# Performance work log

Measured on AMD Instinct MI355X. Metric: run time of the kernel, lower is better.

## Reference

```python
import jax, jax.numpy as jnp
import numpy as np

B, F, O = 4096, 16384, 256
MANTISSA_BITS = 23  # flip only mantissa bits to keep values finite


def setup_inputs() -> dict:
    key = jax.random.key(0)
    k1, k2, k3, k4 = jax.random.split(key, 4)
    x = jax.random.normal(k1, (B, F), dtype=jnp.float32)
    W = jax.random.normal(k2, (F, O), dtype=jnp.float32) * 0.02
    b = jnp.zeros((O,), dtype=jnp.float32)
    bitswap_coeff = jnp.ones((), dtype=jnp.float32)  # scalar 'bitswap_coeff' weight
    # uniform categorical over flattened features == uniform randint
    idx = jax.random.randint(k3, (B,), 0, F, dtype=jnp.int32)
    bit_positions = jax.random.randint(k4, (B,), 0, MANTISSA_BITS, dtype=jnp.int32)
    return {"x": x, "W": W, "b": b, "bitswap_coeff": bitswap_coeff,
            "idx": idx, "bit_positions": bit_positions}


def _bit_flip(g, bit_positions):
    # SimulateSwap: flip one mantissa bit of the float32 representation
    gi = jax.lax.bitcast_convert_type(g, jnp.int32)
    gi = gi ^ (jnp.int32(1) << bit_positions)
    return jax.lax.bitcast_convert_type(gi, jnp.float32)


def reference(x, W, b, bitswap_coeff, idx, bit_positions):
    rows = jnp.arange(x.shape[0])
    # gather_nd(batch_dims=1): one element per batch row
    g = x[rows, idx]                              # [B]
    updates = _bit_flip(g, bit_positions) - g     # swap_sim(x) - x
    # tensor_scatter_nd_update onto zeros, scaled by bitswap coefficient
    pert = jnp.zeros_like(x).at[rows, idx].set(updates) * bitswap_coeff
    # wrapped layer: Dense
    return (x + pert) @ W + b
```

## Files before the change

### kernel.cpp

```cpp
#include <hip/hip_runtime.h>

#define M_DIM 4096
#define K_DIM 16384
#define N_DIM 256

typedef __bf16 bf16x8 __attribute__((ext_vector_type(8)));
typedef float f32x4 __attribute__((ext_vector_type(4)));
typedef unsigned short us4 __attribute__((ext_vector_type(4)));
typedef unsigned short us8 __attribute__((ext_vector_type(8)));

__device__ __forceinline__ unsigned short f2bf(float f) {
  unsigned int u = __float_as_uint(f);
  u += 0x7fffu + ((u >> 16) & 1u);
  return (unsigned short)(u >> 16);
}

__global__ __launch_bounds__(256) void wt_kernel(const float* __restrict__ W,
                                                 unsigned short* __restrict__ Wt) {
  __shared__ float tile[64][65];
  const int k0 = blockIdx.x * 64, n0 = blockIdx.y * 64;
  const int t = threadIdx.x;
#pragma unroll
  for (int r = 0; r < 4; ++r) {
    int idx4 = r * 256 + t;
    int kr = idx4 >> 4, c4 = idx4 & 15;
    f32x4 v = *(const f32x4*)(W + (size_t)(k0 + kr) * N_DIM + n0 + c4 * 4);
#pragma unroll
    for (int j = 0; j < 4; ++j) tile[kr][c4 * 4 + j] = v[j];
  }
  __syncthreads();
#pragma unroll
  for (int r = 0; r < 4; ++r) {
    int nr = (t >> 4) + r * 16, k4 = t & 15;
    us4 o;
#pragma unroll
    for (int j = 0; j < 4; ++j) o[j] = f2bf(tile[k4 * 4 + j][nr]);
    *(us4*)(Wt + (size_t)(n0 + nr) * K_DIM + k0 + k4 * 4) = o;
  }
}

__global__ __launch_bounds__(512) void gemm_kernel(const float* __restrict__ x,
                                                   const unsigned short* __restrict__ Wt,
                                                   unsigned short* __restrict__ part,
                                                   int kslice) {
  __shared__ unsigned short As[128 * 68];
  __shared__ unsigned short Bs[256 * 64];

  const int t = threadIdx.x;
  const int l = t & 63;
  const int w = t >> 6;
  const int wm = w >> 2, wn = w & 3;
  const int la = l & 15, q = l >> 4;
  const int m0 = blockIdx.x * 128;
  const int kbase = blockIdx.y * kslice;

  f32x4 acc[4][4];
  const f32x4 zero = {0.f, 0.f, 0.f, 0.f};
#pragma unroll
  for (int i = 0; i < 4; ++i)
#pragma unroll
    for (int j = 0; j < 4; ++j) acc[i][j] = zero;

  const int niter = kslice / 64;
  for (int it = 0; it < niter; ++it) {
    const int k0 = kbase + it * 64;

#pragma unroll
    for (int c = 0; c < 4; ++c) {
      int nb = w * 32 + c * 8;
      const unsigned short* g = Wt + (size_t)(nb + (l & 7)) * K_DIM + k0 + ((l >> 3) * 8);
      unsigned short* lp = &Bs[nb * 64];
      __builtin_amdgcn_global_load_lds((const __attribute__((address_space(1))) void*)g,
                                       (__attribute__((address_space(3))) void*)lp, 16, 0, 0);
    }

#pragma unroll
    for (int r = 0; r < 4; ++r) {
      int idx4 = r * 512 + t;
      int row = idx4 >> 4, c4 = idx4 & 15;
      f32x4 v = *(const f32x4*)(x + (size_t)(m0 + row) * K_DIM + k0 + c4 * 4);
      us4 o;
      o[0] = f2bf(v[0]); o[1] = f2bf(v[1]); o[2] = f2bf(v[2]); o[3] = f2bf(v[3]);
      *(us4*)(&As[row * 68 + c4 * 4]) = o;
    }
    __syncthreads();

#pragma unroll
    for (int ks = 0; ks < 2; ++ks) {
      const int kb = ks * 32 + q * 8;
      union Frag { bf16x8 v; us4 h[2]; us8 o; };
      Frag a[4], b[4];
#pragma unroll
      for (int i = 0; i < 4; ++i) {
        int ml = wm * 64 + i * 16 + la;
        int off = ml * 68 + kb;
        a[i].h[0] = *(const us4*)(&As[off]);
        a[i].h[1] = *(const us4*)(&As[off + 4]);
      }
#pragma unroll
      for (int j = 0; j < 4; ++j) {
        int n = wn * 64 + j * 16 + la;
        int off = (n >> 3) * 512 + (kb >> 3) * 64 + (n & 7) * 8;
        b[j].o = *(const us8*)(&Bs[off]);
      }
#pragma unroll
      for (int i = 0; i < 4; ++i)
#pragma unroll
        for (int j = 0; j < 4; ++j)
          acc[i][j] = __builtin_amdgcn_mfma_f32_16x16x32_bf16(a[i].v, b[j].v, acc[i][j], 0, 0, 0);
    }
    __syncthreads();
  }

  unsigned short* pbase = part + (size_t)blockIdx.y * ((size_t)M_DIM * N_DIM);
#pragma unroll
  for (int i = 0; i < 4; ++i) {
    int r0 = m0 + wm * 64 + i * 16 + q * 4;
#pragma unroll
    for (int j = 0; j < 4; ++j) {
      int c = wn * 64 + j * 16 + la;
#pragma unroll
      for (int r = 0; r < 4; ++r)
        pbase[(size_t)(r0 + r) * N_DIM + c] = f2bf(acc[i][j][r]);
    }
  }
}

__global__ __launch_bounds__(256) void reduce_kernel(const unsigned short* __restrict__ part,
                                                     int S,
                                                     const float* __restrict__ x,
                                                     const float* __restrict__ W,
                                                     const float* __restrict__ bvec,
                                                     const float* __restrict__ coeffp,
                                                     const int* __restrict__ idx,
                                                     const int* __restrict__ bp,
                                                     float* __restrict__ out) {
  const int row = blockIdx.x;
  const int o = threadIdx.x;
  const int iv = idx[row];
  const float g = x[(size_t)row * K_DIM + iv];
  const int bits = __float_as_int(g) ^ (1 << bp[row]);
  const float upd = __int_as_float(bits) - g;
  const float coeff = coeffp[0];
  const size_t off = (size_t)row * N_DIM + o;
  float sum = 0.f;
  for (int s = 0; s < S; ++s)
    sum += __uint_as_float(((unsigned int)part[(size_t)s * ((size_t)M_DIM * N_DIM) + off]) << 16);
  out[off] = sum + coeff * upd * W[(size_t)iv * N_DIM + o] + bvec[o];
}

extern "C" void kernel_launch(void* const* d_in, const int* in_sizes, int n_in,
                              void* d_out, int out_size, void* d_ws, size_t ws_size,
                              hipStream_t stream) {
  const float* x = (const float*)d_in[0];
  const float* W = (const float*)d_in[1];
  const float* b = (const float*)d_in[2];
  const float* coeff = (const float*)d_in[3];
  const int* idx = (const int*)d_in[4];
  const int* bp = (const int*)d_in[5];
  float* out = (float*)d_out;

  unsigned short* Wt = (unsigned short*)d_ws;
  const size_t wt_bytes = (size_t)K_DIM * N_DIM * 2;
  int S = 8;
  while (S > 1 && wt_bytes + (size_t)S * M_DIM * N_DIM * 2 > ws_size) S >>= 1;
  unsigned short* part = (unsigned short*)((char*)d_ws + wt_bytes);

  hipLaunchKernelGGL(wt_kernel, dim3(K_DIM / 64, N_DIM / 64), dim3(256), 0, stream, W, Wt);
  hipLaunchKernelGGL(gemm_kernel, dim3(M_DIM / 128, S), dim3(512), 0, stream,
                     x, Wt, part, K_DIM / S);
  hipLaunchKernelGGL(reduce_kernel, dim3(M_DIM), dim3(256), 0, stream,
                     part, S, x, W, b, coeff, idx, bp, out);
}
```

Before: 415.3 us.

## Shrink GEMM tile to 64 rows with 4 waves, raise split-K to 16

The GEMM block tile drops from 128x256 with 8 waves to 64x256 with 4 waves. The grid grows to 64x16 blocks with a fixed split-K of 16, and launch bounds now allow 3 blocks per CU, aiming for more parallelism and occupancy. The LDS A tile is padded to a stride of 72 so each A fragment loads as a single 16-byte read, and native __bf16 conversions replace the manual rounding. In exchange, W is reloaded into LDS twice as often, and the partial buffer doubles in size, which adds reduce traffic. The workspace-size check that used to pick S was removed, so the code may overflow a small workspace.

Result: slower. 435.4 us (+4.8%).

```diff
diff --git a/kernel.cpp b/kernel.cpp
--- a/kernel.cpp
+++ b/kernel.cpp
@@ -3,11 +3,12 @@
 #define M_DIM 4096
 #define K_DIM 16384
 #define N_DIM 256
+#define SPLIT 16
 
 typedef __bf16 bf16x8 __attribute__((ext_vector_type(8)));
+typedef __bf16 bf16x4 __attribute__((ext_vector_type(4)));
 typedef float f32x4 __attribute__((ext_vector_type(4)));
 typedef unsigned short us4 __attribute__((ext_vector_type(4)));
-typedef unsigned short us8 __attribute__((ext_vector_type(8)));
 
 __device__ __forceinline__ unsigned short f2bf(float f) {
   unsigned int u = __float_as_uint(f);
@@ -16,7 +17,7 @@
 }
 
 __global__ __launch_bounds__(256) void wt_kernel(const float* __restrict__ W,
-                                                 unsigned short* __restrict__ Wt) {
+                                                 __bf16* __restrict__ Wt) {
   __shared__ float tile[64][65];
   const int k0 = blockIdx.x * 64, n0 = blockIdx.y * 64;
   const int t = threadIdx.x;
@@ -32,26 +33,25 @@
 #pragma unroll
   for (int r = 0; r < 4; ++r) {
     int nr = (t >> 4) + r * 16, k4 = t & 15;
-    us4 o;
+    bf16x4 o;
 #pragma unroll
-    for (int j = 0; j < 4; ++j) o[j] = f2bf(tile[k4 * 4 + j][nr]);
-    *(us4*)(Wt + (size_t)(n0 + nr) * K_DIM + k0 + k4 * 4) = o;
+    for (int j = 0; j < 4; ++j) o[j] = (__bf16)tile[k4 * 4 + j][nr];
+    *(bf16x4*)(Wt + (size_t)(n0 + nr) * K_DIM + k0 + k4 * 4) = o;
   }
 }
 
-__global__ __launch_bounds__(512) void gemm_kernel(const float* __restrict__ x,
-                                                   const unsigned short* __restrict__ Wt,
-                                                   unsigned short* __restrict__ part,
-                                                   int kslice) {
-  __shared__ unsigned short As[128 * 68];
-  __shared__ unsigned short Bs[256 * 64];
+__global__ __launch_bounds__(256, 3) void gemm_kernel(const float* __restrict__ x,
+                                                      const __bf16* __restrict__ Wt,
+                                                      __bf16* __restrict__ part,
+                                                      int kslice) {
+  __shared__ __bf16 As[64 * 72];
+  __shared__ __bf16 Bs[256 * 64];
 
   const int t = threadIdx.x;
   const int l = t & 63;
   const int w = t >> 6;
-  const int wm = w >> 2, wn = w & 3;
   const int la = l & 15, q = l >> 4;
-  const int m0 = blockIdx.x * 128;
+  const int m0 = blockIdx.x * 64;
   const int kbase = blockIdx.y * kslice;
 
   f32x4 acc[4][4];
@@ -61,73 +61,65 @@
 #pragma unroll
     for (int j = 0; j < 4; ++j) acc[i][j] = zero;
 
-  const int niter = kslice / 64;
+  const int niter = kslice >> 6;
   for (int it = 0; it < niter; ++it) {
     const int k0 = kbase + it * 64;
 
 #pragma unroll
-    for (int c = 0; c < 4; ++c) {
-      int nb = w * 32 + c * 8;
-      const unsigned short* g = Wt + (size_t)(nb + (l & 7)) * K_DIM + k0 + ((l >> 3) * 8);
-      unsigned short* lp = &Bs[nb * 64];
+    for (int c = 0; c < 8; ++c) {
+      int nb = w * 64 + c * 8;
+      const __bf16* g = Wt + (size_t)(nb + (l & 7)) * K_DIM + k0 + ((l >> 3) * 8);
+      __bf16* lp = &Bs[nb * 64];
       __builtin_amdgcn_global_load_lds((const __attribute__((address_space(1))) void*)g,
                                        (__attribute__((address_space(3))) void*)lp, 16, 0, 0);
     }
 
 #pragma unroll
     for (int r = 0; r < 4; ++r) {
-      int idx4 = r * 512 + t;
+      int idx4 = r * 256 + t;
       int row = idx4 >> 4, c4 = idx4 & 15;
       f32x4 v = *(const f32x4*)(x + (size_t)(m0 + row) * K_DIM + k0 + c4 * 4);
-      us4 o;
-      o[0] = f2bf(v[0]); o[1] = f2bf(v[1]); o[2] = f2bf(v[2]); o[3] = f2bf(v[3]);
-      *(us4*)(&As[row * 68 + c4 * 4]) = o;
+      bf16x4 o = {(__bf16)v[0], (__bf16)v[1], (__bf16)v[2], (__bf16)v[3]};
+      *(bf16x4*)(&As[row * 72 + c4 * 4]) = o;
     }
     __syncthreads();
 
 #pragma unroll
     for (int ks = 0; ks < 2; ++ks) {
       const int kb = ks * 32 + q * 8;
-      union Frag { bf16x8 v; us4 h[2]; us8 o; };
-      Frag a[4], b[4];
+      bf16x8 a[4], b[4];
 #pragma unroll
-      for (int i = 0; i < 4; ++i) {
-        int ml = wm * 64 + i * 16 + la;
-        int off = ml * 68 + kb;
-        a[i].h[0] = *(const us4*)(&As[off]);
-        a[i].h[1] = *(const us4*)(&As[off + 4]);
-      }
+      for (int i = 0; i < 4; ++i)
+        a[i] = *(const bf16x8*)(&As[(i * 16 + la) * 72 + kb]);
 #pragma unroll
       for (int j = 0; j < 4; ++j) {
-        int n = wn * 64 + j * 16 + la;
-        int off = (n >> 3) * 512 + (kb >> 3) * 64 + (n & 7) * 8;
-        b[j].o = *(const us8*)(&Bs[off]);
+        int n = w * 64 + j * 16 + la;
+        b[j] = *(const bf16x8*)(&Bs[(n >> 3) * 512 + (kb >> 3) * 64 + (n & 7) * 8]);
       }
 #pragma unroll
       for (int i = 0; i < 4; ++i)
 #pragma unroll
         for (int j = 0; j < 4; ++j)
-          acc[i][j] = __builtin_amdgcn_mfma_f32_16x16x32_bf16(a[i].v, b[j].v, acc[i][j], 0, 0, 0);
+          acc[i][j] = __builtin_amdgcn_mfma_f32_16x16x32_bf16(a[i], b[j], acc[i][j], 0, 0, 0);
     }
     __syncthreads();
   }
 
-  unsigned short* pbase = part + (size_t)blockIdx.y * ((size_t)M_DIM * N_DIM);
+  __bf16* pbase = part + (size_t)blockIdx.y * ((size_t)M_DIM * N_DIM);
 #pragma unroll
   for (int i = 0; i < 4; ++i) {
-    int r0 = m0 + wm * 64 + i * 16 + q * 4;
+    int r0 = m0 + i * 16 + q * 4;
 #pragma unroll
     for (int j = 0; j < 4; ++j) {
-      int c = wn * 64 + j * 16 + la;
+      int c = w * 64 + j * 16 + la;
 #pragma unroll
       for (int r = 0; r < 4; ++r)
-        pbase[(size_t)(r0 + r) * N_DIM + c] = f2bf(acc[i][j][r]);
+        pbase[(size_t)(r0 + r) * N_DIM + c] = (__bf16)acc[i][j][r];
     }
   }
 }
 
-__global__ __launch_bounds__(256) void reduce_kernel(const unsigned short* __restrict__ part,
-                                                     int S,
+__global__ __launch_bounds__(256) void reduce_kernel(const __bf16* __restrict__ part,
                                                      const float* __restrict__ x,
                                                      const float* __restrict__ W,
                                                      const float* __restrict__ bvec,
@@ -144,8 +136,9 @@
   const float coeff = coeffp[0];
   const size_t off = (size_t)row * N_DIM + o;
   float sum = 0.f;
-  for (int s = 0; s < S; ++s)
-    sum += __uint_as_float(((unsigned int)part[(size_t)s * ((size_t)M_DIM * N_DIM) + off]) << 16);
+#pragma unroll
+  for (int s = 0; s < SPLIT; ++s)
+    sum += (float)part[(size_t)s * ((size_t)M_DIM * N_DIM) + off];
   out[off] = sum + coeff * upd * W[(size_t)iv * N_DIM + o] + bvec[o];
 }
 
@@ -160,15 +153,13 @@
   const int* bp = (const int*)d_in[5];
   float* out = (float*)d_out;
 
-  unsigned short* Wt = (unsigned short*)d_ws;
+  __bf16* Wt = (__bf16*)d_ws;
   const size_t wt_bytes = (size_t)K_DIM * N_DIM * 2;
-  int S = 8;
-  while (S > 1 && wt_bytes + (size_t)S * M_DIM * N_DIM * 2 > ws_size) S >>= 1;
-  unsigned short* part = (unsigned short*)((char*)d_ws + wt_bytes);
+  __bf16* part = (__bf16*)((char*)d_ws + wt_bytes);
 
   hipLaunchKernelGGL(wt_kernel, dim3(K_DIM / 64, N_DIM / 64), dim3(256), 0, stream, W, Wt);
-  hipLaunchKernelGGL(gemm_kernel, dim3(M_DIM / 128, S), dim3(512), 0, stream,
-                     x, Wt, part, K_DIM / S);
+  hipLaunchKernelGGL(gemm_kernel, dim3(M_DIM / 64, SPLIT), dim3(256), 0, stream,
+                     x, Wt, part, K_DIM / SPLIT);
   hipLaunchKernelGGL(reduce_kernel, dim3(M_DIM), dim3(256), 0, stream,
-                     part, S, x, W, b, coeff, idx, bp, out);
+                     part, x, W, b, coeff, idx, bp, out);
 }
```
